# Kernel optimization log

Hardware: AMD Instinct MI355X
Metric: run time of the kernel (lower is better)

Reference implementation:

```python
import jax, jax.numpy as jnp
import numpy as np

HEADS = 8
DIM_HEAD = 32
DIM = HEADS * DIM_HEAD  # 256
B, H, W = 2, 256, 256


def _dw2d(x, wgt):
    # depthwise 3x3 conv, NCHW, weight (C,1,3,3)
    return jax.lax.conv_general_dilated(
        x, wgt, window_strides=(1, 1), padding='SAME',
        feature_group_count=x.shape[1],
        dimension_numbers=('NCHW', 'OIHW', 'NCHW'))


def setup_inputs() -> dict:
    key = jax.random.key(0)
    ks = jax.random.split(key, 20)
    def kaiming(k, shape, fan_in):
        return jax.random.normal(k, shape, jnp.float32) * np.sqrt(2.0 / fan_in)
    inp = {}
    inp['x_in'] = jax.random.normal(ks[0], (B, H, W, DIM), jnp.float32)
    # shared depthwise weights (heads,1,3,3), kaiming_normal fan_in=9
    names = ['qw1', 'qw2', 'qw3', 'kw1', 'kw2', 'kw3', 'vw1', 'vw2', 'vw3']
    for i, n in enumerate(names):
        inp[n] = kaiming(ks[1 + i], (HEADS, 1, 3, 3), 9)
    # pos_emb: two depthwise convs dim->dim with bias
    inp['pos_w1'] = kaiming(ks[10], (DIM, 1, 3, 3), 9)
    inp['pos_b1'] = jnp.zeros((DIM,), jnp.float32)
    inp['pos_w2'] = kaiming(ks[11], (DIM, 1, 3, 3), 9)
    inp['pos_b2'] = jnp.zeros((DIM,), jnp.float32)
    # conv1d heads->heads kernel 3
    inp['conv1d_w'] = kaiming(ks[12], (HEADS, HEADS, 3), HEADS * 3)
    inp['conv1d_b'] = jnp.zeros((HEADS,), jnp.float32)
    inp['rescale'] = jnp.ones((HEADS, 1, 1), jnp.float32)
    inp['rescale2'] = jnp.ones((HEADS, 1, 1), jnp.float32)
    inp['proj_w'] = kaiming(ks[13], (DIM, DIM), DIM)  # (out,in) torch layout
    inp['proj_b'] = jnp.zeros((DIM,), jnp.float32)
    return inp


def reference(x_in, qw1, qw2, qw3, kw1, kw2, kw3, vw1, vw2, vw3,
              pos_w1, pos_b1, pos_w2, pos_b2, conv1d_w, conv1d_b,
              rescale, rescale2, proj_w, proj_b):
    b, h, w, c = x_in.shape
    heads = rescale.shape[0]
    dim_head = c // heads
    x = jnp.transpose(x_in, (0, 3, 1, 2))  # NCHW
    # positional embedding: dwconv -> gelu(exact) -> dwconv
    t = _dw2d(x, pos_w1) + pos_b1[None, :, None, None]
    t = jax.nn.gelu(t, approximate=False)
    t = _dw2d(t, pos_w2) + pos_b2[None, :, None, None]
    x = x + t

    def chain(x, w1, w2, w3):
        for wgt in (w1, w2, w3):
            x = _dw2d(x, jnp.repeat(wgt, dim_head, axis=0))
        return x

    q = chain(x, qw1, qw2, qw3)
    k = chain(x, kw1, kw2, kw3)
    v = chain(x, vw1, vw2, vw3)
    # (b,c,h,w) -> (b,heads,dim_head,hw) ; channel = head*dim_head + d
    q = q.reshape(b, heads, dim_head, h * w)
    k = k.reshape(b, heads, dim_head, h * w)
    v = v.reshape(b, heads, dim_head, h * w)
    eps = 1e-12
    q = q / jnp.maximum(jnp.linalg.norm(q, axis=-1, keepdims=True), eps)
    k = k / jnp.maximum(jnp.linalg.norm(k, axis=-1, keepdims=True), eps)
    # channel attention: k @ q^T -> (b,heads,dim_head,dim_head)
    attn = jnp.einsum('bhdn,bhen->bhde', k, q)
    # pooled v -> conv1d over dim_head length, channels = heads
    y = v.mean(axis=-1)  # (b,heads,dim_head)
    attn_v = jax.lax.conv_general_dilated(
        y, conv1d_w, window_strides=(1,), padding='SAME',
        dimension_numbers=('NCH', 'OIH', 'NCH')) + conv1d_b[None, :, None]
    diag = attn_v[..., :, None] * jnp.eye(dim_head, dtype=attn.dtype)
    attn = attn * rescale[None] + diag * rescale2[None]
    attn = jax.nn.softmax(attn, axis=-1)
    out = jnp.einsum('bhde,bhen->bhdn', attn, v)  # (b,heads,dim_head,hw)
    out = jnp.transpose(out, (0, 3, 1, 2)).reshape(b, h * w, c)
    out = out @ proj_w.T + proj_b
    return out.reshape(b, h, w, c)
```

## Files before the change

kernel.cpp:

```cpp
#include <hip/hip_runtime.h>
#include <stdint.h>
#include <math.h>


using u16 = unsigned short;
using u32 = unsigned int;

typedef __bf16 bf16x8_t __attribute__((ext_vector_type(8)));
typedef float f32x4_t __attribute__((ext_vector_type(4)));

__device__ __forceinline__ float bf2f(u16 v) {
  u32 u = ((u32)v) << 16;
  return __builtin_bit_cast(float, u);
}
__device__ __forceinline__ u16 f2bf(float f) {
  u32 u = __builtin_bit_cast(u32, f);
  u32 r = u + 0x7fffu + ((u >> 16) & 1u);
  return (u16)(r >> 16);
}
__device__ __forceinline__ void unpack8(uint4 u, float f[8]) {
  f[0] = bf2f((u16)(u.x & 0xffffu)); f[1] = bf2f((u16)(u.x >> 16));
  f[2] = bf2f((u16)(u.y & 0xffffu)); f[3] = bf2f((u16)(u.y >> 16));
  f[4] = bf2f((u16)(u.z & 0xffffu)); f[5] = bf2f((u16)(u.z >> 16));
  f[6] = bf2f((u16)(u.w & 0xffffu)); f[7] = bf2f((u16)(u.w >> 16));
}
__device__ __forceinline__ uint4 pack8(const u16 o[8]) {
  uint4 v;
  v.x = (u32)o[0] | ((u32)o[1] << 16);
  v.y = (u32)o[2] | ((u32)o[3] << 16);
  v.z = (u32)o[4] | ((u32)o[5] << 16);
  v.w = (u32)o[6] | ((u32)o[7] << 16);
  return v;
}

__global__ __launch_bounds__(256) void posemb_kernel(
    const float* __restrict__ xin, u16* __restrict__ x2,
    const float* __restrict__ w1g, const float* __restrict__ b1g,
    const float* __restrict__ w2g, const float* __restrict__ b2g) {
  const int t = threadIdx.x;
  const int o = t & 3;
  const int bz = blockIdx.z;
  const int cg = bz & 7;
  const int b = bz >> 3;
  const int x0 = blockIdx.x * 16;
  const int y0 = blockIdx.y * 8;
  const int c0 = cg * 32 + o * 8;

  __shared__ __align__(16) u16 Abuf[240 * 32];
  __shared__ __align__(16) u16 Bbuf[180 * 32];

  for (int i = t; i < 240 * 4; i += 256) {
    const int px = i >> 2, oo = i & 3;
    const int lx = px % 20, ly = px / 20;
    const int gx = x0 - 2 + lx, gy = y0 - 2 + ly;
    u16 ov[8];
    if (gx >= 0 && gx < 256 && gy >= 0 && gy < 256) {
      const float* p = xin + ((size_t)((b << 16) + (gy << 8) + gx)) * 256 + cg * 32 + oo * 8;
      const float4 r0 = *reinterpret_cast<const float4*>(p);
      const float4 r1 = *reinterpret_cast<const float4*>(p + 4);
      ov[0] = f2bf(r0.x); ov[1] = f2bf(r0.y); ov[2] = f2bf(r0.z); ov[3] = f2bf(r0.w);
      ov[4] = f2bf(r1.x); ov[5] = f2bf(r1.y); ov[6] = f2bf(r1.z); ov[7] = f2bf(r1.w);
    } else {
#pragma unroll
      for (int j = 0; j < 8; ++j) ov[j] = 0;
    }
    *reinterpret_cast<uint4*>(Abuf + px * 32 + oo * 8) = pack8(ov);
  }
  __syncthreads();

  {
    float w[72], bi[8];
#pragma unroll
    for (int j = 0; j < 8; ++j) {
#pragma unroll
      for (int k = 0; k < 9; ++k) w[j * 9 + k] = w1g[(c0 + j) * 9 + k];
      bi[j] = b1g[c0 + j];
    }
    for (int i = t; i < 180 * 4; i += 256) {
      const int px = i >> 2;
      const int sx = px % 18, sy = px / 18;
      const int gx = x0 - 1 + sx, gy = y0 - 1 + sy;
      const bool inb = (gx >= 0 && gx < 256 && gy >= 0 && gy < 256);
      float a[8];
#pragma unroll
      for (int j = 0; j < 8; ++j) a[j] = bi[j];
#pragma unroll
      for (int ky = 0; ky < 3; ++ky)
#pragma unroll
        for (int kx = 0; kx < 3; ++kx) {
          float f[8];
          unpack8(*reinterpret_cast<const uint4*>(
                      Abuf + ((sy + ky) * 20 + sx + kx) * 32 + o * 8), f);
#pragma unroll
          for (int j = 0; j < 8; ++j) a[j] = fmaf(w[j * 9 + ky * 3 + kx], f[j], a[j]);
        }
      u16 ov[8];
#pragma unroll
      for (int j = 0; j < 8; ++j) {
        const float g = 0.5f * a[j] * (1.0f + erff(a[j] * 0.70710678118654752f));
        ov[j] = inb ? f2bf(g) : (u16)0;
      }
      *reinterpret_cast<uint4*>(Bbuf + px * 32 + o * 8) = pack8(ov);
    }
  }
  __syncthreads();

  {
    float w[72], bi[8];
#pragma unroll
    for (int j = 0; j < 8; ++j) {
#pragma unroll
      for (int k = 0; k < 9; ++k) w[j * 9 + k] = w2g[(c0 + j) * 9 + k];
      bi[j] = b2g[c0 + j];
    }
    for (int i = t; i < 128 * 4; i += 256) {
      const int px = i >> 2;
      const int sx = px & 15, sy = px >> 4;
      float a[8];
#pragma unroll
      for (int j = 0; j < 8; ++j) a[j] = bi[j];
#pragma unroll
      for (int ky = 0; ky < 3; ++ky)
#pragma unroll
        for (int kx = 0; kx < 3; ++kx) {
          float f[8];
          unpack8(*reinterpret_cast<const uint4*>(
                      Bbuf + ((sy + ky) * 18 + sx + kx) * 32 + o * 8), f);
#pragma unroll
          for (int j = 0; j < 8; ++j) a[j] = fmaf(w[j * 9 + ky * 3 + kx], f[j], a[j]);
        }
      float xr[8];
      unpack8(*reinterpret_cast<const uint4*>(
                  Abuf + ((sy + 2) * 20 + sx + 2) * 32 + o * 8), xr);
      u16 ov[8];
#pragma unroll
      for (int j = 0; j < 8; ++j) ov[j] = f2bf(a[j] + xr[j]);
      u16* dst = x2 + ((size_t)((b << 16) + ((y0 + sy) << 8) + x0 + sx)) * 256 + cg * 32 + o * 8;
      *reinterpret_cast<uint4*>(dst) = pack8(ov);
    }
  }
}

template <int RED>
__global__ __launch_bounds__(256) void chain3_kernel(
    const u16* __restrict__ in, u16* __restrict__ out,
    const float* __restrict__ w1g, const float* __restrict__ w2g,
    const float* __restrict__ w3g, float* __restrict__ red) {
  const int t = threadIdx.x;
  const int o = t & 3;
  const int bz = blockIdx.z;
  const int h = bz & 7;
  const int b = bz >> 3;
  const int x0 = blockIdx.x * 16;
  const int y0 = blockIdx.y * 8;

  __shared__ __align__(16) u16 Abuf[308 * 32];
  __shared__ __align__(16) u16 Bbuf[240 * 32];
  __shared__ float rbuf[32];
  if (t < 32) rbuf[t] = 0.f;

  float w1[9], w2[9], w3[9];
#pragma unroll
  for (int k = 0; k < 9; ++k) {
    w1[k] = w1g[h * 9 + k];
    w2[k] = w2g[h * 9 + k];
    w3[k] = w3g[h * 9 + k];
  }

  for (int i = t; i < 308 * 4; i += 256) {
    const int px = i >> 2, oo = i & 3;
    const int lx = px % 22, ly = px / 22;
    const int gx = x0 - 3 + lx, gy = y0 - 3 + ly;
    uint4 v = {0, 0, 0, 0};
    if (gx >= 0 && gx < 256 && gy >= 0 && gy < 256)
      v = *reinterpret_cast<const uint4*>(
          in + ((size_t)((b << 16) + (gy << 8) + gx)) * 256 + h * 32 + oo * 8);
    *reinterpret_cast<uint4*>(Abuf + px * 32 + oo * 8) = v;
  }
  __syncthreads();

  for (int i = t; i < 240 * 4; i += 256) {
    const int px = i >> 2;
    const int sx = px % 20, sy = px / 20;
    const int gx = x0 - 2 + sx, gy = y0 - 2 + sy;
    const bool inb = (gx >= 0 && gx < 256 && gy >= 0 && gy < 256);
    float a[8] = {0, 0, 0, 0, 0, 0, 0, 0};
#pragma unroll
    for (int ky = 0; ky < 3; ++ky)
#pragma unroll
      for (int kx = 0; kx < 3; ++kx) {
        float f[8];
        unpack8(*reinterpret_cast<const uint4*>(
                    Abuf + ((sy + ky) * 22 + sx + kx) * 32 + o * 8), f);
#pragma unroll
        for (int j = 0; j < 8; ++j) a[j] = fmaf(w1[ky * 3 + kx], f[j], a[j]);
      }
    u16 ov[8];
#pragma unroll
    for (int j = 0; j < 8; ++j) ov[j] = inb ? f2bf(a[j]) : (u16)0;
    *reinterpret_cast<uint4*>(Bbuf + px * 32 + o * 8) = pack8(ov);
  }
  __syncthreads();

  for (int i = t; i < 180 * 4; i += 256) {
    const int px = i >> 2;
    const int sx = px % 18, sy = px / 18;
    const int gx = x0 - 1 + sx, gy = y0 - 1 + sy;
    const bool inb = (gx >= 0 && gx < 256 && gy >= 0 && gy < 256);
    float a[8] = {0, 0, 0, 0, 0, 0, 0, 0};
#pragma unroll
    for (int ky = 0; ky < 3; ++ky)
#pragma unroll
      for (int kx = 0; kx < 3; ++kx) {
        float f[8];
        unpack8(*reinterpret_cast<const uint4*>(
                    Bbuf + ((sy + ky) * 20 + sx + kx) * 32 + o * 8), f);
#pragma unroll
        for (int j = 0; j < 8; ++j) a[j] = fmaf(w2[ky * 3 + kx], f[j], a[j]);
      }
    u16 ov[8];
#pragma unroll
    for (int j = 0; j < 8; ++j) ov[j] = inb ? f2bf(a[j]) : (u16)0;
    *reinterpret_cast<uint4*>(Abuf + px * 32 + o * 8) = pack8(ov);
  }
  __syncthreads();

  float racc[8] = {0, 0, 0, 0, 0, 0, 0, 0};
  for (int i = t; i < 128 * 4; i += 256) {
    const int px = i >> 2;
    const int sx = px & 15, sy = px >> 4;
    float a[8] = {0, 0, 0, 0, 0, 0, 0, 0};
#pragma unroll
    for (int ky = 0; ky < 3; ++ky)
#pragma unroll
      for (int kx = 0; kx < 3; ++kx) {
        float f[8];
        unpack8(*reinterpret_cast<const uint4*>(
                    Abuf + ((sy + ky) * 18 + sx + kx) * 32 + o * 8), f);
#pragma unroll
        for (int j = 0; j < 8; ++j) a[j] = fmaf(w3[ky * 3 + kx], f[j], a[j]);
      }
    u16 ov[8];
#pragma unroll
    for (int j = 0; j < 8; ++j) {
      ov[j] = f2bf(a[j]);
      const float rv = bf2f(ov[j]);
      if (RED == 1) racc[j] = fmaf(rv, rv, racc[j]);
      if (RED == 2) racc[j] += rv;
    }
    u16* dst = out + ((size_t)((b << 16) + ((y0 + sy) << 8) + x0 + sx)) * 256 + h * 32 + o * 8;
    *reinterpret_cast<uint4*>(dst) = pack8(ov);
  }
  __syncthreads();
#pragma unroll
  for (int j = 0; j < 8; ++j) atomicAdd(&rbuf[o * 8 + j], racc[j]);
  __syncthreads();
  if (t < 32) atomicAdd(&red[b * 256 + h * 32 + t], rbuf[t]);
}

__global__ __launch_bounds__(256) void kchain_gram_kernel(
    const u16* __restrict__ in, const u16* __restrict__ q3,
    const float* __restrict__ w1g, const float* __restrict__ w2g,
    const float* __restrict__ w3g, float* __restrict__ G, float* __restrict__ sqk) {
  const int t = threadIdx.x;
  const int o = t & 3;
  const int bz = blockIdx.z;
  const int h = bz & 7;
  const int b = bz >> 3;
  const int x0 = blockIdx.x * 16;
  const int y0 = blockIdx.y * 8;

  __shared__ __align__(16) u16 Abuf[308 * 32];
  __shared__ __align__(16) u16 Bbuf[240 * 32];
  __shared__ __align__(16) u16 K3s[32 * 132];
  __shared__ __align__(16) u16 Q3s[32 * 132];
  __shared__ float rbuf[32];
  if (t < 32) rbuf[t] = 0.f;

  float w1[9], w2[9], w3[9];
#pragma unroll
  for (int k = 0; k < 9; ++k) {
    w1[k] = w1g[h * 9 + k];
    w2[k] = w2g[h * 9 + k];
    w3[k] = w3g[h * 9 + k];
  }

  for (int i = t; i < 308 * 4; i += 256) {
    const int px = i >> 2, oo = i & 3;
    const int lx = px % 22, ly = px / 22;
    const int gx = x0 - 3 + lx, gy = y0 - 3 + ly;
    uint4 v = {0, 0, 0, 0};
    if (gx >= 0 && gx < 256 && gy >= 0 && gy < 256)
      v = *reinterpret_cast<const uint4*>(
          in + ((size_t)((b << 16) + (gy << 8) + gx)) * 256 + h * 32 + oo * 8);
    *reinterpret_cast<uint4*>(Abuf + px * 32 + oo * 8) = v;
  }
  __syncthreads();

  for (int i = t; i < 240 * 4; i += 256) {
    const int px = i >> 2;
    const int sx = px % 20, sy = px / 20;
    const int gx = x0 - 2 + sx, gy = y0 - 2 + sy;
    const bool inb = (gx >= 0 && gx < 256 && gy >= 0 && gy < 256);
    float a[8] = {0, 0, 0, 0, 0, 0, 0, 0};
#pragma unroll
    for (int ky = 0; ky < 3; ++ky)
#pragma unroll
      for (int kx = 0; kx < 3; ++kx) {
        float f[8];
        unpack8(*reinterpret_cast<const uint4*>(
                    Abuf + ((sy + ky) * 22 + sx + kx) * 32 + o * 8), f);
#pragma unroll
        for (int j = 0; j < 8; ++j) a[j] = fmaf(w1[ky * 3 + kx], f[j], a[j]);
      }
    u16 ov[8];
#pragma unroll
    for (int j = 0; j < 8; ++j) ov[j] = inb ? f2bf(a[j]) : (u16)0;
    *reinterpret_cast<uint4*>(Bbuf + px * 32 + o * 8) = pack8(ov);
  }
  __syncthreads();

  for (int i = t; i < 180 * 4; i += 256) {
    const int px = i >> 2;
    const int sx = px % 18, sy = px / 18;
    const int gx = x0 - 1 + sx, gy = y0 - 1 + sy;
    const bool inb = (gx >= 0 && gx < 256 && gy >= 0 && gy < 256);
    float a[8] = {0, 0, 0, 0, 0, 0, 0, 0};
#pragma unroll
    for (int ky = 0; ky < 3; ++ky)
#pragma unroll
      for (int kx = 0; kx < 3; ++kx) {
        float f[8];
        unpack8(*reinterpret_cast<const uint4*>(
                    Bbuf + ((sy + ky) * 20 + sx + kx) * 32 + o * 8), f);
#pragma unroll
        for (int j = 0; j < 8; ++j) a[j] = fmaf(w2[ky * 3 + kx], f[j], a[j]);
      }
    u16 ov[8];
#pragma unroll
    for (int j = 0; j < 8; ++j) ov[j] = inb ? f2bf(a[j]) : (u16)0;
    *reinterpret_cast<uint4*>(Abuf + px * 32 + o * 8) = pack8(ov);
  }
  __syncthreads();

  float racc[8] = {0, 0, 0, 0, 0, 0, 0, 0};
  for (int i = t; i < 128 * 4; i += 256) {
    const int px = i >> 2;
    const int sx = px & 15, sy = px >> 4;
    float a[8] = {0, 0, 0, 0, 0, 0, 0, 0};
#pragma unroll
    for (int ky = 0; ky < 3; ++ky)
#pragma unroll
      for (int kx = 0; kx < 3; ++kx) {
        float f[8];
        unpack8(*reinterpret_cast<const uint4*>(
                    Abuf + ((sy + ky) * 18 + sx + kx) * 32 + o * 8), f);
#pragma unroll
        for (int j = 0; j < 8; ++j) a[j] = fmaf(w3[ky * 3 + kx], f[j], a[j]);
      }
#pragma unroll
    for (int j = 0; j < 8; ++j) {
      const u16 kb16 = f2bf(a[j]);
      const float kv = bf2f(kb16);
      K3s[(o * 8 + j) * 132 + px] = kb16;
      racc[j] = fmaf(kv, kv, racc[j]);
    }
    const uint4 uq = *reinterpret_cast<const uint4*>(
        q3 + ((size_t)((b << 16) + ((y0 + sy) << 8) + x0 + sx)) * 256 + h * 32 + o * 8);
    Q3s[(o * 8 + 0) * 132 + px] = (u16)(uq.x & 0xffffu);
    Q3s[(o * 8 + 1) * 132 + px] = (u16)(uq.x >> 16);
    Q3s[(o * 8 + 2) * 132 + px] = (u16)(uq.y & 0xffffu);
    Q3s[(o * 8 + 3) * 132 + px] = (u16)(uq.y >> 16);
    Q3s[(o * 8 + 4) * 132 + px] = (u16)(uq.z & 0xffffu);
    Q3s[(o * 8 + 5) * 132 + px] = (u16)(uq.z >> 16);
    Q3s[(o * 8 + 6) * 132 + px] = (u16)(uq.w & 0xffffu);
    Q3s[(o * 8 + 7) * 132 + px] = (u16)(uq.w >> 16);
  }
  __syncthreads();
#pragma unroll
  for (int j = 0; j < 8; ++j) atomicAdd(&rbuf[o * 8 + j], racc[j]);
  __syncthreads();
  if (t < 32) atomicAdd(&sqk[b * 256 + h * 32 + t], rbuf[t]);

  const int wave = t >> 6;
  const int lane = t & 63;
  const int quad = lane >> 4;
  const int l15 = lane & 15;
  const int d0 = (wave & 1) * 16;
  const int e0 = (wave >> 1) * 16;
  f32x4_t acc = {0.f, 0.f, 0.f, 0.f};
#pragma unroll
  for (int kb = 0; kb < 4; ++kb) {
    const bf16x8_t av = *reinterpret_cast<const bf16x8_t*>(
        &K3s[(d0 + l15) * 132 + kb * 32 + quad * 8]);
    const bf16x8_t bv = *reinterpret_cast<const bf16x8_t*>(
        &Q3s[(e0 + l15) * 132 + kb * 32 + quad * 8]);
    acc = __builtin_amdgcn_mfma_f32_16x16x32_bf16(av, bv, acc, 0, 0, 0);
  }
  float* Gp = G + (size_t)((b * 8 + h) * 32) * 32;
#pragma unroll
  for (int r = 0; r < 4; ++r)
    atomicAdd(&Gp[(d0 + quad * 4 + r) * 32 + e0 + l15], acc[r]);
}

__global__ __launch_bounds__(256) void attn_kernel(
    const float* __restrict__ G, const float* __restrict__ sqq,
    const float* __restrict__ sqk, const float* __restrict__ vsum,
    const float* __restrict__ cw, const float* __restrict__ cb,
    const float* __restrict__ rs1, const float* __restrict__ rs2,
    float* __restrict__ attn) {
  const int b = blockIdx.x;
  const int t = threadIdx.x;
  const int h = t >> 5;
  const int d = t & 31;
  __shared__ float vm[8][34];
  __shared__ float nq[256];
  vm[h][d + 1] = vsum[b * 256 + t] * (1.0f / 65536.0f);
  if (t < 8) { vm[t][0] = 0.f; vm[t][33] = 0.f; }
  nq[t] = fmaxf(sqrtf(sqq[b * 256 + t]), 1e-12f);
  __syncthreads();

  float av = cb[h];
#pragma unroll
  for (int i = 0; i < 8; ++i)
#pragma unroll
    for (int tau = 0; tau < 3; ++tau)
      av = fmaf(cw[h * 24 + i * 3 + tau], vm[i][d + tau], av);

  const float nk = fmaxf(sqrtf(sqk[b * 256 + t]), 1e-12f);
  const float rsc = rs1[h];
  const float rsc2 = rs2[h];
  const float* Gp = G + (size_t)((b * 8 + h) * 32 + d) * 32;
  float L[32];
#pragma unroll
  for (int e = 0; e < 32; ++e) {
    float l = Gp[e] * rsc / (nk * nq[h * 32 + e]);
    if (e == d) l += av * rsc2;
    L[e] = l;
  }
  float mx = L[0];
#pragma unroll
  for (int e = 1; e < 32; ++e) mx = fmaxf(mx, L[e]);
  float s = 0.f;
#pragma unroll
  for (int e = 0; e < 32; ++e) {
    L[e] = expf(L[e] - mx);
    s += L[e];
  }
  const float inv = 1.0f / s;
  float* Ap = attn + (size_t)((b * 8 + h) * 32 + d) * 32;
#pragma unroll
  for (int e = 0; e < 32; ++e) Ap[e] = L[e] * inv;
}

__global__ __launch_bounds__(256) void mbuild_kernel(
    const float* __restrict__ attn, const float* __restrict__ pw,
    u16* __restrict__ M) {
  const int bid = blockIdx.x;
  const int b = bid >> 3;
  const int h = bid & 7;
  const int t = threadIdx.x;
  __shared__ float at[32][33];
#pragma unroll
  for (int i = 0; i < 4; ++i) {
    const int idx = t * 4 + i;
    at[idx >> 5][idx & 31] = attn[(size_t)(b * 8 + h) * 1024 + idx];
  }
  __syncthreads();
  float pwf[32];
#pragma unroll
  for (int dd = 0; dd < 32; ++dd) pwf[dd] = pw[(size_t)t * 256 + h * 32 + dd];
  u16* Mp = M + (size_t)b * 65536 + (size_t)t * 256 + h * 32;
#pragma unroll
  for (int e = 0; e < 32; ++e) {
    float s = 0.f;
#pragma unroll
    for (int dd = 0; dd < 32; ++dd) s = fmaf(pwf[dd], at[dd][e], s);
    Mp[e] = f2bf(s);
  }
}

__global__ __launch_bounds__(256) void gemm_kernel(
    const u16* __restrict__ V, const u16* __restrict__ Mm,
    const float* __restrict__ pb, float* __restrict__ out) {
  const int m0 = blockIdx.x * 128;
  const int n0 = blockIdx.y * 64;
  const int b = m0 >> 16;
  const u16* Mb = Mm + (size_t)b * 65536;

  __shared__ __align__(16) u16 As[128][72];
  __shared__ __align__(16) u16 Bs[64][72];

  const int t = threadIdx.x;
  const int wave = t >> 6;
  const int lane = t & 63;
  const int quad = lane >> 4;
  const int l15 = lane & 15;

  f32x4_t acc[2][4];
#pragma unroll
  for (int mt = 0; mt < 2; ++mt)
#pragma unroll
    for (int nt = 0; nt < 4; ++nt) acc[mt][nt] = {0.f, 0.f, 0.f, 0.f};

  for (int k0 = 0; k0 < 256; k0 += 64) {
#pragma unroll
    for (int i = 0; i < 4; ++i) {
      const int id = t + 256 * i;
      const int row = id >> 3;
      const int c8 = id & 7;
      *reinterpret_cast<uint4*>(&As[row][c8 * 8]) = *reinterpret_cast<const uint4*>(
          &V[(size_t)(m0 + row) * 256 + k0 + c8 * 8]);
    }
#pragma unroll
    for (int i = 0; i < 2; ++i) {
      const int id = t + 256 * i;
      const int row = id >> 3;
      const int c8 = id & 7;
      *reinterpret_cast<uint4*>(&Bs[row][c8 * 8]) = *reinterpret_cast<const uint4*>(
          &Mb[(size_t)(n0 + row) * 256 + k0 + c8 * 8]);
    }
    __syncthreads();
#pragma unroll
    for (int ks = 0; ks < 2; ++ks) {
      bf16x8_t af[2], bfv[4];
#pragma unroll
      for (int mt = 0; mt < 2; ++mt)
        af[mt] = *reinterpret_cast<const bf16x8_t*>(
            &As[wave * 32 + mt * 16 + l15][ks * 32 + quad * 8]);
#pragma unroll
      for (int nt = 0; nt < 4; ++nt)
        bfv[nt] = *reinterpret_cast<const bf16x8_t*>(
            &Bs[nt * 16 + l15][ks * 32 + quad * 8]);
#pragma unroll
      for (int mt = 0; mt < 2; ++mt)
#pragma unroll
        for (int nt = 0; nt < 4; ++nt)
          acc[mt][nt] =
              __builtin_amdgcn_mfma_f32_16x16x32_bf16(af[mt], bfv[nt], acc[mt][nt], 0, 0, 0);
    }
    __syncthreads();
  }

#pragma unroll
  for (int nt = 0; nt < 4; ++nt) {
    const int col = n0 + nt * 16 + l15;
    const float pbf = pb[col];
#pragma unroll
    for (int mt = 0; mt < 2; ++mt) {
#pragma unroll
      for (int r = 0; r < 4; ++r) {
        const int m = m0 + wave * 32 + mt * 16 + quad * 4 + r;
        out[(size_t)m * 256 + col] = acc[mt][nt][r] + pbf;
      }
    }
  }
}

extern "C" void kernel_launch(void* const* d_in, const int* in_sizes, int n_in,
                              void* d_out, int out_size, void* d_ws, size_t ws_size,
                              hipStream_t stream) {
  const float* x_in = (const float*)d_in[0];
  const float* qw1 = (const float*)d_in[1];
  const float* qw2 = (const float*)d_in[2];
  const float* qw3 = (const float*)d_in[3];
  const float* kw1 = (const float*)d_in[4];
  const float* kw2 = (const float*)d_in[5];
  const float* kw3 = (const float*)d_in[6];
  const float* vw1 = (const float*)d_in[7];
  const float* vw2 = (const float*)d_in[8];
  const float* vw3 = (const float*)d_in[9];
  const float* posw1 = (const float*)d_in[10];
  const float* posb1 = (const float*)d_in[11];
  const float* posw2 = (const float*)d_in[12];
  const float* posb2 = (const float*)d_in[13];
  const float* cw = (const float*)d_in[14];
  const float* cb = (const float*)d_in[15];
  const float* rs1 = (const float*)d_in[16];
  const float* rs2 = (const float*)d_in[17];
  const float* pw = (const float*)d_in[18];
  const float* pb = (const float*)d_in[19];

  char* ws = (char*)d_ws;
  const size_t SLOT = 67108864;
  u16* S0 = (u16*)(ws);
  u16* S1 = (u16*)(ws + SLOT);
  u16* D0 = (u16*)d_out;
  char* SM = ws + 2 * SLOT;
  float* G = (float*)(SM);
  float* sqq = (float*)(SM + 65536);
  float* sqk = (float*)(SM + 67584);
  float* vsum = (float*)(SM + 69632);
  float* attn = (float*)(SM + 71680);
  u16* Mm = (u16*)(SM + 137216);

  hipMemsetAsync(SM, 0, 71680, stream);

  const dim3 tgrid(16, 32, 16);
  posemb_kernel<<<tgrid, 256, 0, stream>>>(x_in, S0, posw1, posb1, posw2, posb2);
  chain3_kernel<1><<<tgrid, 256, 0, stream>>>(S0, D0, qw1, qw2, qw3, sqq);
  kchain_gram_kernel<<<tgrid, 256, 0, stream>>>(S0, D0, kw1, kw2, kw3, G, sqk);
  chain3_kernel<2><<<tgrid, 256, 0, stream>>>(S0, S1, vw1, vw2, vw3, vsum);
  attn_kernel<<<2, 256, 0, stream>>>(G, sqq, sqk, vsum, cw, cb, rs1, rs2, attn);
  mbuild_kernel<<<16, 256, 0, stream>>>(attn, pw, Mm);
  gemm_kernel<<<dim3(1024, 4), 256, 0, stream>>>(S1, Mm, pb, (float*)d_out);
}
```

Before: 943.2 us.

## Compose 3x3 depthwise chains into 7x7 kernels and fuse q/k/v interior tiles

Precomputes a single 7x7 depthwise kernel per head for each q/k/v chain by convolving the three 3x3 weights, then runs one fused kernel over interior tiles. That kernel reads the input tile once and computes q, k, v, the norms, the v sums and the k·q^T Gram via MFMA. Border tiles, where zero padding between stages breaks the composition, still use the original three-stage kernels on a reduced grid. This removes the intermediate bf16 rounding between stages and the triple reads of the input, at the cost of small numeric differences.

Result: faster. 878.5 us (-6.9%).

```diff
diff --git a/kernel.cpp b/kernel.cpp
--- a/kernel.cpp
+++ b/kernel.cpp
@@ -31,6 +31,36 @@
   v.z = (u32)o[4] | ((u32)o[5] << 16);
   v.w = (u32)o[6] | ((u32)o[7] << 16);
   return v;
+}
+
+__global__ __launch_bounds__(64) void compose_kernel(
+    const float* __restrict__ qw1, const float* __restrict__ qw2,
+    const float* __restrict__ qw3, const float* __restrict__ kw1,
+    const float* __restrict__ kw2, const float* __restrict__ kw3,
+    const float* __restrict__ vw1, const float* __restrict__ vw2,
+    const float* __restrict__ vw3, float* __restrict__ Wc) {
+  const int t = threadIdx.x;
+  if (t >= 24) return;
+  const int h = t / 3, c = t % 3;
+  const float* w1 = (c == 0 ? qw1 : c == 1 ? kw1 : vw1) + h * 9;
+  const float* w2 = (c == 0 ? qw2 : c == 1 ? kw2 : vw2) + h * 9;
+  const float* w3 = (c == 0 ? qw3 : c == 1 ? kw3 : vw3) + h * 9;
+  float w12[25];
+  for (int i = 0; i < 25; ++i) w12[i] = 0.f;
+  for (int ky = 0; ky < 3; ++ky)
+    for (int kx = 0; kx < 3; ++kx)
+      for (int ly = 0; ly < 3; ++ly)
+        for (int lx = 0; lx < 3; ++lx)
+          w12[(ky + ly) * 5 + kx + lx] += w2[ky * 3 + kx] * w1[ly * 3 + lx];
+  float we[49];
+  for (int i = 0; i < 49; ++i) we[i] = 0.f;
+  for (int my = 0; my < 3; ++my)
+    for (int mx = 0; mx < 3; ++mx)
+      for (int ey = 0; ey < 5; ++ey)
+        for (int ex = 0; ex < 5; ++ex)
+          we[(my + ey) * 7 + mx + ex] += w3[my * 3 + mx] * w12[ey * 5 + ex];
+  float* dst = Wc + (h * 3 + c) * 49;
+  for (int i = 0; i < 49; ++i) dst[i] = we[i];
 }
 
 __global__ __launch_bounds__(256) void posemb_kernel(
@@ -141,7 +171,178 @@
   }
 }
 
-template <int RED>
+__global__ __launch_bounds__(256) void qkv_fused_kernel(
+    const u16* __restrict__ x2, u16* __restrict__ v3out,
+    const float* __restrict__ Wc, float* __restrict__ G,
+    float* __restrict__ sqq, float* __restrict__ sqk,
+    float* __restrict__ vsum) {
+  const int t = threadIdx.x;
+  const int o = t & 3;
+  const int sx = (t >> 2) & 15;
+  const int yg = t >> 6;
+  const int bz = blockIdx.z;
+  const int h = bz & 7;
+  const int b = bz >> 3;
+  const int x0 = (blockIdx.x + 1) * 16;
+  const int y0 = (blockIdx.y + 1) * 8;
+
+  __shared__ __align__(16) u16 Abuf[308 * 32];
+  __shared__ float rbuf[96];
+  if (t < 96) rbuf[t] = 0.f;
+
+  for (int i = t; i < 308 * 4; i += 256) {
+    const int px = i >> 2, oo = i & 3;
+    const int lx = px % 22, ly = px / 22;
+    const int gx = x0 - 3 + lx, gy = y0 - 3 + ly;
+    *reinterpret_cast<uint4*>(Abuf + px * 32 + oo * 8) =
+        *reinterpret_cast<const uint4*>(
+            x2 + ((size_t)((b << 16) + (gy << 8) + gx)) * 256 + h * 32 + oo * 8);
+  }
+  __syncthreads();
+
+  const float* Wq = Wc + (h * 3 + 0) * 49;
+  const float* Wk = Wc + (h * 3 + 1) * 49;
+  const float* Wv = Wc + (h * 3 + 2) * 49;
+
+  float aq[2][8], ak[2][8], av2[2][8];
+#pragma unroll
+  for (int r = 0; r < 2; ++r)
+#pragma unroll
+    for (int j = 0; j < 8; ++j) { aq[r][j] = 0.f; ak[r][j] = 0.f; av2[r][j] = 0.f; }
+
+  const int ty0 = yg * 2;
+  const u16* Arow0 = Abuf + (ty0 * 22 + sx) * 32 + o * 8;
+
+  {
+    const u16* Ar = Arow0;
+#pragma unroll
+    for (int jx = 0; jx < 7; ++jx) {
+      float f[8];
+      unpack8(*reinterpret_cast<const uint4*>(Ar + jx * 32), f);
+      const float wq = Wq[jx], wk = Wk[jx], wv = Wv[jx];
+#pragma unroll
+      for (int j = 0; j < 8; ++j) {
+        aq[0][j] = fmaf(wq, f[j], aq[0][j]);
+        ak[0][j] = fmaf(wk, f[j], ak[0][j]);
+        av2[0][j] = fmaf(wv, f[j], av2[0][j]);
+      }
+    }
+  }
+#pragma unroll 1
+  for (int iy = 1; iy <= 6; ++iy) {
+    const u16* Ar = Arow0 + iy * (22 * 32);
+    const float* wq0 = Wq + iy * 7;
+    const float* wk0 = Wk + iy * 7;
+    const float* wv0 = Wv + iy * 7;
+#pragma unroll
+    for (int jx = 0; jx < 7; ++jx) {
+      float f[8];
+      unpack8(*reinterpret_cast<const uint4*>(Ar + jx * 32), f);
+      float w;
+      w = wq0[jx];
+#pragma unroll
+      for (int j = 0; j < 8; ++j) aq[0][j] = fmaf(w, f[j], aq[0][j]);
+      w = wq0[jx - 7];
+#pragma unroll
+      for (int j = 0; j < 8; ++j) aq[1][j] = fmaf(w, f[j], aq[1][j]);
+      w = wk0[jx];
+#pragma unroll
+      for (int j = 0; j < 8; ++j) ak[0][j] = fmaf(w, f[j], ak[0][j]);
+      w = wk0[jx - 7];
+#pragma unroll
+      for (int j = 0; j < 8; ++j) ak[1][j] = fmaf(w, f[j], ak[1][j]);
+      w = wv0[jx];
+#pragma unroll
+      for (int j = 0; j < 8; ++j) av2[0][j] = fmaf(w, f[j], av2[0][j]);
+      w = wv0[jx - 7];
+#pragma unroll
+      for (int j = 0; j < 8; ++j) av2[1][j] = fmaf(w, f[j], av2[1][j]);
+    }
+  }
+  {
+    const u16* Ar = Arow0 + 7 * (22 * 32);
+#pragma unroll
+    for (int jx = 0; jx < 7; ++jx) {
+      float f[8];
+      unpack8(*reinterpret_cast<const uint4*>(Ar + jx * 32), f);
+      const float wq = Wq[42 + jx], wk = Wk[42 + jx], wv = Wv[42 + jx];
+#pragma unroll
+      for (int j = 0; j < 8; ++j) {
+        aq[1][j] = fmaf(wq, f[j], aq[1][j]);
+        ak[1][j] = fmaf(wk, f[j], ak[1][j]);
+        av2[1][j] = fmaf(wv, f[j], av2[1][j]);
+      }
+    }
+  }
+
+  __syncthreads();
+
+  u16* K3s = Abuf;
+  u16* Q3s = Abuf + 32 * 132;
+
+  float rq[8], rk[8], rv[8];
+#pragma unroll
+  for (int j = 0; j < 8; ++j) { rq[j] = 0.f; rk[j] = 0.f; rv[j] = 0.f; }
+#pragma unroll
+  for (int ry = 0; ry < 2; ++ry) {
+    const int px = (ty0 + ry) * 16 + sx;
+    u16 ov[8];
+#pragma unroll
+    for (int j = 0; j < 8; ++j) {
+      const u16 qb = f2bf(aq[ry][j]);
+      Q3s[(o * 8 + j) * 132 + px] = qb;
+      const float qf = bf2f(qb);
+      rq[j] = fmaf(qf, qf, rq[j]);
+      const u16 kb = f2bf(ak[ry][j]);
+      K3s[(o * 8 + j) * 132 + px] = kb;
+      const float kf = bf2f(kb);
+      rk[j] = fmaf(kf, kf, rk[j]);
+      ov[j] = f2bf(av2[ry][j]);
+      rv[j] += bf2f(ov[j]);
+    }
+    u16* dst = v3out + ((size_t)((b << 16) + ((y0 + ty0 + ry) << 8) + x0 + sx)) * 256 + h * 32 + o * 8;
+    *reinterpret_cast<uint4*>(dst) = pack8(ov);
+  }
+#pragma unroll
+  for (int j = 0; j < 8; ++j) {
+    atomicAdd(&rbuf[o * 8 + j], rq[j]);
+    atomicAdd(&rbuf[32 + o * 8 + j], rk[j]);
+    atomicAdd(&rbuf[64 + o * 8 + j], rv[j]);
+  }
+  __syncthreads();
+
+  const int wave = t >> 6;
+  const int lane = t & 63;
+  const int quad = lane >> 4;
+  const int l15 = lane & 15;
+  const int d0 = (wave & 1) * 16;
+  const int e0 = (wave >> 1) * 16;
+  f32x4_t acc = {0.f, 0.f, 0.f, 0.f};
+#pragma unroll
+  for (int kb = 0; kb < 4; ++kb) {
+    const bf16x8_t avf = *reinterpret_cast<const bf16x8_t*>(
+        &K3s[(d0 + l15) * 132 + kb * 32 + quad * 8]);
+    const bf16x8_t bvf = *reinterpret_cast<const bf16x8_t*>(
+        &Q3s[(e0 + l15) * 132 + kb * 32 + quad * 8]);
+    acc = __builtin_amdgcn_mfma_f32_16x16x32_bf16(avf, bvf, acc, 0, 0, 0);
+  }
+  float* Gp = G + (size_t)((b * 8 + h) * 32) * 32;
+#pragma unroll
+  for (int r = 0; r < 4; ++r)
+    atomicAdd(&Gp[(d0 + quad * 4 + r) * 32 + e0 + l15], acc[r]);
+
+  if (t < 32) atomicAdd(&sqq[b * 256 + h * 32 + t], rbuf[t]);
+  else if (t < 64) atomicAdd(&sqk[b * 256 + h * 32 + (t - 32)], rbuf[t]);
+  else if (t < 96) atomicAdd(&vsum[b * 256 + h * 32 + (t - 64)], rbuf[t]);
+}
+
+__device__ __forceinline__ void border_map(int bi, int& bx, int& by) {
+  if (bi < 16) { bx = bi; by = 0; }
+  else if (bi < 32) { bx = bi - 16; by = 31; }
+  else { const int e = bi - 32; by = 1 + (e >> 1); bx = (e & 1) * 15; }
+}
+
+template <int RED, int BORDER>
 __global__ __launch_bounds__(256) void chain3_kernel(
     const u16* __restrict__ in, u16* __restrict__ out,
     const float* __restrict__ w1g, const float* __restrict__ w2g,
@@ -151,8 +352,10 @@
   const int bz = blockIdx.z;
   const int h = bz & 7;
   const int b = bz >> 3;
-  const int x0 = blockIdx.x * 16;
-  const int y0 = blockIdx.y * 8;
+  int bx = blockIdx.x, by = blockIdx.y;
+  if (BORDER) border_map(blockIdx.x, bx, by);
+  const int x0 = bx * 16;
+  const int y0 = by * 8;
 
   __shared__ __align__(16) u16 Abuf[308 * 32];
   __shared__ __align__(16) u16 Bbuf[240 * 32];
@@ -258,6 +461,7 @@
   if (t < 32) atomicAdd(&red[b * 256 + h * 32 + t], rbuf[t]);
 }
 
+template <int BORDER>
 __global__ __launch_bounds__(256) void kchain_gram_kernel(
     const u16* __restrict__ in, const u16* __restrict__ q3,
     const float* __restrict__ w1g, const float* __restrict__ w2g,
@@ -267,8 +471,10 @@
   const int bz = blockIdx.z;
   const int h = bz & 7;
   const int b = bz >> 3;
-  const int x0 = blockIdx.x * 16;
-  const int y0 = blockIdx.y * 8;
+  int bx = blockIdx.x, by = blockIdx.y;
+  if (BORDER) border_map(blockIdx.x, bx, by);
+  const int x0 = bx * 16;
+  const int y0 = by * 8;
 
   __shared__ __align__(16) u16 Abuf[308 * 32];
   __shared__ __align__(16) u16 Bbuf[240 * 32];
@@ -593,14 +799,23 @@
   float* vsum = (float*)(SM + 69632);
   float* attn = (float*)(SM + 71680);
   u16* Mm = (u16*)(SM + 137216);
+  float* Wc = (float*)(SM + 399360);
 
   hipMemsetAsync(SM, 0, 71680, stream);
+
+  compose_kernel<<<1, 64, 0, stream>>>(qw1, qw2, qw3, kw1, kw2, kw3,
+                                       vw1, vw2, vw3, Wc);
 
   const dim3 tgrid(16, 32, 16);
   posemb_kernel<<<tgrid, 256, 0, stream>>>(x_in, S0, posw1, posb1, posw2, posb2);
-  chain3_kernel<1><<<tgrid, 256, 0, stream>>>(S0, D0, qw1, qw2, qw3, sqq);
-  kchain_gram_kernel<<<tgrid, 256, 0, stream>>>(S0, D0, kw1, kw2, kw3, G, sqk);
-  chain3_kernel<2><<<tgrid, 256, 0, stream>>>(S0, S1, vw1, vw2, vw3, vsum);
+
+  qkv_fused_kernel<<<dim3(14, 30, 16), 256, 0, stream>>>(S0, S1, Wc, G, sqq, sqk, vsum);
+
+  const dim3 bgrid(92, 1, 16);
+  chain3_kernel<1, 1><<<bgrid, 256, 0, stream>>>(S0, D0, qw1, qw2, qw3, sqq);
+  kchain_gram_kernel<1><<<bgrid, 256, 0, stream>>>(S0, D0, kw1, kw2, kw3, G, sqk);
+  chain3_kernel<2, 1><<<bgrid, 256, 0, stream>>>(S0, S1, vw1, vw2, vw3, vsum);
+
   attn_kernel<<<2, 256, 0, stream>>>(G, sqq, sqk, vsum, cw, cb, rs1, rs2, attn);
   mbuild_kernel<<<16, 256, 0, stream>>>(attn, pw, Mm);
   gemm_kernel<<<dim3(1024, 4), 256, 0, stream>>>(S1, Mm, pb, (float*)d_out);
```

## Compose three depthwise convs into one 7x7 MFMA conv fused for q/k/v

Applied to the files above, without the earlier changes.

Precomputes the composed 7x7 kernel of each three-conv chain and stores it as banded Toeplitz tables with hi/lo bf16 split. A new fused kernel then computes q, k and v for all interior tiles in one pass using MFMA. The same pass accumulates the norms, the v sum and the k·q Gram matrix, which removes three separate chain passes and repeated reads of the input. Border tiles still go through the original chain kernels with remapped grids, because zero padding between stages makes the composed kernel inexact there. Risks include small numerical differences from composing the kernels in bf16 with a hi/lo split, and the use of spare output memory for the table.

Measured after the change: 1.027 ms. +8.9%, slower.

```diff
diff --git a/kernel.cpp b/kernel.cpp
--- a/kernel.cpp
+++ b/kernel.cpp
@@ -31,6 +31,62 @@
   v.z = (u32)o[4] | ((u32)o[5] << 16);
   v.w = (u32)o[6] | ((u32)o[7] << 16);
   return v;
+}
+__device__ __forceinline__ uint2 pack4(const u16 o[4]) {
+  uint2 v;
+  v.x = (u32)o[0] | ((u32)o[1] << 16);
+  v.y = (u32)o[2] | ((u32)o[3] << 16);
+  return v;
+}
+
+__global__ __launch_bounds__(256) void compose_kernel(
+    const float* __restrict__ qw1, const float* __restrict__ qw2,
+    const float* __restrict__ qw3, const float* __restrict__ kw1,
+    const float* __restrict__ kw2, const float* __restrict__ kw3,
+    const float* __restrict__ vw1, const float* __restrict__ vw2,
+    const float* __restrict__ vw3, u16* __restrict__ Tab) {
+  __shared__ float Wf[24][49];
+  const int t = threadIdx.x;
+  if (t < 24) {
+    const int h = t / 3, c = t % 3;
+    const float* w1 = (c == 0 ? qw1 : c == 1 ? kw1 : vw1) + h * 9;
+    const float* w2 = (c == 0 ? qw2 : c == 1 ? kw2 : vw2) + h * 9;
+    const float* w3 = (c == 0 ? qw3 : c == 1 ? kw3 : vw3) + h * 9;
+    float w12[25];
+    for (int i = 0; i < 25; ++i) w12[i] = 0.f;
+    for (int ky = 0; ky < 3; ++ky)
+      for (int kx = 0; kx < 3; ++kx)
+        for (int ly = 0; ly < 3; ++ly)
+          for (int lx = 0; lx < 3; ++lx)
+            w12[(ky + ly) * 5 + kx + lx] += w2[ky * 3 + kx] * w1[ly * 3 + lx];
+    float we[49];
+    for (int i = 0; i < 49; ++i) we[i] = 0.f;
+    for (int my = 0; my < 3; ++my)
+      for (int mx = 0; mx < 3; ++mx)
+        for (int ey = 0; ey < 5; ++ey)
+          for (int ex = 0; ex < 5; ++ex)
+            we[(my + ey) * 7 + mx + ex] += w3[my * 3 + mx] * w12[ey * 5 + ex];
+    for (int i = 0; i < 49; ++i) Wf[t][i] = we[i];
+  }
+  __syncthreads();
+  for (int e = t; e < 21504; e += 256) {
+    const int lane = e & 63;
+    int r1 = e >> 6;
+    const int dy = r1 % 7;
+    int r2 = r1 / 7;
+    const int part = r2 & 1;
+    const int hc = r2 >> 1;
+    const int x = lane & 15, q = lane >> 4;
+    u16 ov[8];
+#pragma unroll
+    for (int j = 0; j < 8; ++j) {
+      const int d = q * 8 + j - x;
+      const float wv = (d >= 0 && d < 7) ? Wf[hc][dy * 7 + d] : 0.f;
+      const u16 hb = f2bf(wv);
+      ov[j] = (part == 0) ? hb : f2bf(wv - bf2f(hb));
+    }
+    *reinterpret_cast<uint4*>(Tab + (size_t)e * 8) = pack8(ov);
+  }
 }
 
 __global__ __launch_bounds__(256) void posemb_kernel(
@@ -141,7 +197,142 @@
   }
 }
 
-template <int RED>
+__global__ __launch_bounds__(256) void qkv_fused_kernel(
+    const u16* __restrict__ x2, u16* __restrict__ v3out,
+    const u16* __restrict__ Tab, float* __restrict__ G,
+    float* __restrict__ sqq, float* __restrict__ sqk,
+    float* __restrict__ vsum) {
+  const int t = threadIdx.x;
+  const int wave = t >> 6;
+  const int lane = t & 63;
+  const int q = lane >> 4;
+  const int n = lane & 15;
+  const int choff = n >> 3;
+  const int yy = n & 7;
+  const int bz = blockIdx.z;
+  const int h = bz & 7;
+  const int b = bz >> 3;
+  const int x0 = (blockIdx.x + 1) * 16;
+  const int y0 = (blockIdx.y + 1) * 8;
+
+  __shared__ __align__(16) u16 Xt[10768];
+
+  u32* XtW = reinterpret_cast<u32*>(Xt);
+  for (int i = t; i < 520; i += 256) {
+    if (i < 512) {
+      const int ch = i >> 4, row = i & 15;
+      if (row < 14) XtW[ch * 168 + row * 12 + 11] = 0u;
+    } else {
+      XtW[5376 + (i - 512)] = 0u;
+    }
+  }
+
+  for (int px = lane; px < 308; px += 64) {
+    const int ly = px / 22, lx = px - ly * 22;
+    const int gx = x0 - 3 + lx, gy = y0 - 3 + ly;
+    const uint4 v = *reinterpret_cast<const uint4*>(
+        x2 + ((size_t)((b << 16) + (gy << 8) + gx)) * 256 + h * 32 + wave * 8);
+    u16* dst = Xt + (wave * 8) * 336 + ly * 24 + lx;
+    dst[0]    = (u16)(v.x & 0xffffu); dst[336]  = (u16)(v.x >> 16);
+    dst[672]  = (u16)(v.y & 0xffffu); dst[1008] = (u16)(v.y >> 16);
+    dst[1344] = (u16)(v.z & 0xffffu); dst[1680] = (u16)(v.z >> 16);
+    dst[2016] = (u16)(v.w & 0xffffu); dst[2352] = (u16)(v.w >> 16);
+  }
+  __syncthreads();
+
+  f32x4_t acc[3][4];
+#pragma unroll
+  for (int c = 0; c < 3; ++c)
+#pragma unroll
+    for (int pl = 0; pl < 4; ++pl) acc[c][pl] = {0.f, 0.f, 0.f, 0.f};
+
+  const u16* TabL = Tab + (size_t)h * 21504 + (size_t)lane * 8;
+  int rowb[4];
+#pragma unroll
+  for (int pl = 0; pl < 4; ++pl)
+    rowb[pl] = (2 * (wave * 4 + pl) + choff) * 336 + yy * 24 + q * 8;
+
+#pragma unroll
+  for (int dy = 0; dy < 7; ++dy) {
+    bf16x8_t Ah[3], Al[3];
+#pragma unroll
+    for (int c = 0; c < 3; ++c) {
+      Ah[c] = *reinterpret_cast<const bf16x8_t*>(TabL + (size_t)((c * 2 + 0) * 7 + dy) * 512);
+      Al[c] = *reinterpret_cast<const bf16x8_t*>(TabL + (size_t)((c * 2 + 1) * 7 + dy) * 512);
+    }
+#pragma unroll
+    for (int pl = 0; pl < 4; ++pl) {
+      const bf16x8_t Bv = *reinterpret_cast<const bf16x8_t*>(&Xt[rowb[pl] + dy * 24]);
+      acc[0][pl] = __builtin_amdgcn_mfma_f32_16x16x32_bf16(Ah[0], Bv, acc[0][pl], 0, 0, 0);
+      acc[1][pl] = __builtin_amdgcn_mfma_f32_16x16x32_bf16(Ah[1], Bv, acc[1][pl], 0, 0, 0);
+      acc[2][pl] = __builtin_amdgcn_mfma_f32_16x16x32_bf16(Ah[2], Bv, acc[2][pl], 0, 0, 0);
+      acc[0][pl] = __builtin_amdgcn_mfma_f32_16x16x32_bf16(Al[0], Bv, acc[0][pl], 0, 0, 0);
+      acc[1][pl] = __builtin_amdgcn_mfma_f32_16x16x32_bf16(Al[1], Bv, acc[1][pl], 0, 0, 0);
+      acc[2][pl] = __builtin_amdgcn_mfma_f32_16x16x32_bf16(Al[2], Bv, acc[2][pl], 0, 0, 0);
+    }
+  }
+  __syncthreads();
+
+  u16* K3s = Xt;
+  u16* Q3s = Xt + 32 * 132;
+
+  const int masks[5] = {1, 2, 4, 16, 32};
+#pragma unroll
+  for (int pl = 0; pl < 4; ++pl) {
+    const int ch = 2 * (wave * 4 + pl) + choff;
+    float sq = 0.f, sk = 0.f, sv = 0.f;
+    u16 qb[4], kb[4], vb[4];
+#pragma unroll
+    for (int r = 0; r < 4; ++r) {
+      qb[r] = f2bf(acc[0][pl][r]);
+      const float qf = bf2f(qb[r]); sq = fmaf(qf, qf, sq);
+      kb[r] = f2bf(acc[1][pl][r]);
+      const float kf = bf2f(kb[r]); sk = fmaf(kf, kf, sk);
+      vb[r] = f2bf(acc[2][pl][r]);
+      sv += bf2f(vb[r]);
+    }
+    *reinterpret_cast<uint2*>(&Q3s[ch * 132 + yy * 16 + q * 4]) = pack4(qb);
+    *reinterpret_cast<uint2*>(&K3s[ch * 132 + yy * 16 + q * 4]) = pack4(kb);
+    u16* vp = v3out + ((size_t)((b << 16) + ((y0 + yy) << 8) + (x0 + q * 4))) * 256 + h * 32 + ch;
+    vp[0] = vb[0]; vp[256] = vb[1]; vp[512] = vb[2]; vp[768] = vb[3];
+#pragma unroll
+    for (int mi = 0; mi < 5; ++mi) {
+      sq += __shfl_xor(sq, masks[mi]);
+      sk += __shfl_xor(sk, masks[mi]);
+      sv += __shfl_xor(sv, masks[mi]);
+    }
+    if ((lane & 55) == 0) {
+      atomicAdd(&sqq[b * 256 + h * 32 + ch], sq);
+      atomicAdd(&sqk[b * 256 + h * 32 + ch], sk);
+      atomicAdd(&vsum[b * 256 + h * 32 + ch], sv);
+    }
+  }
+  __syncthreads();
+
+  const int d0 = (wave & 1) * 16;
+  const int e0 = (wave >> 1) * 16;
+  f32x4_t ga = {0.f, 0.f, 0.f, 0.f};
+#pragma unroll
+  for (int kb4 = 0; kb4 < 4; ++kb4) {
+    const bf16x8_t avf = *reinterpret_cast<const bf16x8_t*>(
+        &K3s[(d0 + n) * 132 + kb4 * 32 + q * 8]);
+    const bf16x8_t bvf = *reinterpret_cast<const bf16x8_t*>(
+        &Q3s[(e0 + n) * 132 + kb4 * 32 + q * 8]);
+    ga = __builtin_amdgcn_mfma_f32_16x16x32_bf16(avf, bvf, ga, 0, 0, 0);
+  }
+  float* Gp = G + (size_t)((b * 8 + h) * 32) * 32;
+#pragma unroll
+  for (int r = 0; r < 4; ++r)
+    atomicAdd(&Gp[(d0 + q * 4 + r) * 32 + e0 + n], ga[r]);
+}
+
+__device__ __forceinline__ void border_map(int bi, int& bx, int& by) {
+  if (bi < 16) { bx = bi; by = 0; }
+  else if (bi < 32) { bx = bi - 16; by = 31; }
+  else { const int e = bi - 32; by = 1 + (e >> 1); bx = (e & 1) * 15; }
+}
+
+template <int RED, int BORDER>
 __global__ __launch_bounds__(256) void chain3_kernel(
     const u16* __restrict__ in, u16* __restrict__ out,
     const float* __restrict__ w1g, const float* __restrict__ w2g,
@@ -151,8 +342,10 @@
   const int bz = blockIdx.z;
   const int h = bz & 7;
   const int b = bz >> 3;
-  const int x0 = blockIdx.x * 16;
-  const int y0 = blockIdx.y * 8;
+  int bx = blockIdx.x, by = blockIdx.y;
+  if (BORDER) border_map(blockIdx.x, bx, by);
+  const int x0 = bx * 16;
+  const int y0 = by * 8;
 
   __shared__ __align__(16) u16 Abuf[308 * 32];
   __shared__ __align__(16) u16 Bbuf[240 * 32];
@@ -258,6 +451,7 @@
   if (t < 32) atomicAdd(&red[b * 256 + h * 32 + t], rbuf[t]);
 }
 
+template <int BORDER>
 __global__ __launch_bounds__(256) void kchain_gram_kernel(
     const u16* __restrict__ in, const u16* __restrict__ q3,
     const float* __restrict__ w1g, const float* __restrict__ w2g,
@@ -267,8 +461,10 @@
   const int bz = blockIdx.z;
   const int h = bz & 7;
   const int b = bz >> 3;
-  const int x0 = blockIdx.x * 16;
-  const int y0 = blockIdx.y * 8;
+  int bx = blockIdx.x, by = blockIdx.y;
+  if (BORDER) border_map(blockIdx.x, bx, by);
+  const int x0 = bx * 16;
+  const int y0 = by * 8;
 
   __shared__ __align__(16) u16 Abuf[308 * 32];
   __shared__ __align__(16) u16 Bbuf[240 * 32];
@@ -593,14 +789,23 @@
   float* vsum = (float*)(SM + 69632);
   float* attn = (float*)(SM + 71680);
   u16* Mm = (u16*)(SM + 137216);
+  u16* Tab = (u16*)((char*)d_out + 100663296);
 
   hipMemsetAsync(SM, 0, 71680, stream);
+
+  compose_kernel<<<1, 256, 0, stream>>>(qw1, qw2, qw3, kw1, kw2, kw3,
+                                        vw1, vw2, vw3, Tab);
 
   const dim3 tgrid(16, 32, 16);
   posemb_kernel<<<tgrid, 256, 0, stream>>>(x_in, S0, posw1, posb1, posw2, posb2);
-  chain3_kernel<1><<<tgrid, 256, 0, stream>>>(S0, D0, qw1, qw2, qw3, sqq);
-  kchain_gram_kernel<<<tgrid, 256, 0, stream>>>(S0, D0, kw1, kw2, kw3, G, sqk);
-  chain3_kernel<2><<<tgrid, 256, 0, stream>>>(S0, S1, vw1, vw2, vw3, vsum);
+
+  qkv_fused_kernel<<<dim3(14, 30, 16), 256, 0, stream>>>(S0, S1, Tab, G, sqq, sqk, vsum);
+
+  const dim3 bgrid(92, 1, 16);
+  chain3_kernel<1, 1><<<bgrid, 256, 0, stream>>>(S0, D0, qw1, qw2, qw3, sqq);
+  kchain_gram_kernel<1><<<bgrid, 256, 0, stream>>>(S0, D0, kw1, kw2, kw3, G, sqk);
+  chain3_kernel<2, 1><<<bgrid, 256, 0, stream>>>(S0, S1, vw1, vw2, vw3, vsum);
+
   attn_kernel<<<2, 256, 0, stream>>>(G, sqq, sqk, vsum, cw, cb, rs1, rs2, attn);
   mbuild_kernel<<<16, 256, 0, stream>>>(attn, pw, Mm);
   gemm_kernel<<<dim3(1024, 4), 256, 0, stream>>>(S1, Mm, pb, (float*)d_out);
```
